# Optimization experiments

Measured on AMD Instinct MI355X. Metric: run time of the kernel, lower is better.

## Reference

```python
import jax, jax.numpy as jnp
import numpy as np


def _mlp2(x, w1, b1, w2, b2):
    # two-linear MLP with tanh after each layer (Sequential(MLP, activation))
    h = jnp.tanh(x @ w1.T + b1)
    return jnp.tanh(h @ w2.T + b2)


def setup_inputs() -> dict:
    key = jax.random.key(0)
    ks = jax.random.split(key, 12)
    N, K, D, H, C = 20000, 32, 128, 128, 64
    s = 0.1
    return {
        "z": jax.random.normal(ks[0], (N, D), jnp.float32),
        "z_": jax.random.normal(ks[1], (N, K, D), jnp.float32),
        "cur_w1": s * jax.random.normal(ks[2], (H, D), jnp.float32),
        "cur_b1": jax.random.uniform(ks[3], (H,), jnp.float32, -0.1, 0.1),
        "cur_w2": s * jax.random.normal(ks[4], (H, H), jnp.float32),
        "cur_b2": jax.random.uniform(ks[5], (H,), jnp.float32, -0.1, 0.1),
        "nbr_w1": s * jax.random.normal(ks[6], (H, 2 * D), jnp.float32),
        "nbr_b1": jax.random.uniform(ks[7], (H,), jnp.float32, -0.1, 0.1),
        "nbr_w2": s * jax.random.normal(ks[8], (H, H), jnp.float32),
        "nbr_b2": jax.random.uniform(ks[9], (H,), jnp.float32, -0.1, 0.1),
        "out_w": s * jax.random.normal(ks[10], (C, 2 * H), jnp.float32),
        "out_b": jax.random.uniform(ks[11], (C,), jnp.float32, -0.1, 0.1),
    }


def reference(z, z_, cur_w1, cur_b1, cur_w2, cur_b2,
              nbr_w1, nbr_b1, nbr_w2, nbr_b2, out_w, out_b):
    N, K, D = z_.shape
    # current-node branch: [N, H]
    v = _mlp2(z, cur_w1, cur_b1, cur_w2, cur_b2)
    # neighbor branch: repeat z over K, concat with z_ -> [N, K, 2D]
    zc = jnp.concatenate([jnp.broadcast_to(z[:, None, :], (N, K, D)), z_], axis=2)
    vn = _mlp2(zc, nbr_w1, nbr_b1, nbr_w2, nbr_b2)  # [N, K, H]
    v_ = vn.sum(axis=1)  # sum-aggregate over neighbors -> [N, H]
    # output linear on concatenated features -> [N, dim_c]
    dc = jnp.concatenate([v, v_], axis=1) @ out_w.T + out_b
    return dc
```

## Files before the change

### kernel.cpp

```cpp
#include <hip/hip_runtime.h>


typedef __bf16 bf16;
typedef __bf16 bf16x2 __attribute__((ext_vector_type(2)));
typedef __bf16 bf16x4 __attribute__((ext_vector_type(4)));
typedef __bf16 bf16x8 __attribute__((ext_vector_type(8)));
typedef float  f32x4  __attribute__((ext_vector_type(4)));

#define MFMA(a, b, c) __builtin_amdgcn_mfma_f32_16x16x32_bf16((a), (b), (c), 0, 0, 0)

#define C2LOG2E 2.885390081777927f

__device__ __forceinline__ void block_sync_lds() {
    asm volatile("s_waitcnt lgkmcnt(0)\n\ts_barrier" ::: "memory");
}

__device__ __forceinline__ float fast_tanh(float x) {
    float t = __builtin_amdgcn_exp2f(x * C2LOG2E);
    return 1.0f - 2.0f * __builtin_amdgcn_rcpf(t + 1.0f);
}
__device__ __forceinline__ float fast_tanh_fb(float acc, float uc) {
    float t = __builtin_amdgcn_exp2f(__builtin_fmaf(acc, C2LOG2E, uc));
    return 1.0f - 2.0f * __builtin_amdgcn_rcpf(t + 1.0f);
}
__device__ __forceinline__ float tanh_rpart(float acc, float uc) {
    float t = __builtin_amdgcn_exp2f(__builtin_fmaf(acc, C2LOG2E, uc));
    return __builtin_amdgcn_rcpf(t + 1.0f);
}

__device__ __forceinline__ bf16x8 cvt8(f32x4 a, f32x4 b) {
    bf16x8 r;
    r[0] = (bf16)a[0]; r[1] = (bf16)a[1]; r[2] = (bf16)a[2]; r[3] = (bf16)a[3];
    r[4] = (bf16)b[0]; r[5] = (bf16)b[1]; r[6] = (bf16)b[2]; r[7] = (bf16)b[3];
    return r;
}

__device__ __forceinline__ int swz128(int row, int col) {
    int c = (col >> 3) ^ (row & 15);
    return row * 256 + c * 16 + (col & 7) * 2;
}
__device__ __forceinline__ int swz256(int row, int col) {
    int c = (col >> 3) ^ (row & 15);
    return row * 512 + c * 16 + (col & 7) * 2;
}

__device__ __forceinline__ void st_pair(char* base, int off, float a, float b) {
    bf16x2 p = {(bf16)a, (bf16)b};
    *(bf16x2*)(base + off) = p;
}

__global__ __launch_bounds__(256, 2) void nbr_kernel(
    const float* __restrict__ zn, const float* __restrict__ u1,
    const float* __restrict__ w1, const float* __restrict__ w2,
    const float* __restrict__ b2,
    bf16* __restrict__ feat, int NP)
{
    __shared__ char zc_lds[2][32 * 256];
    __shared__ char h1_lds[2][32 * 256];

    const int t = threadIdx.x;
    const int wv = t >> 6, lane = t & 63, g = lane >> 4, li = lane & 15;
    const int hbase = wv * 32;

    bf16x8 w1f[2][4];
#pragma unroll
    for (int ht = 0; ht < 2; ++ht)
#pragma unroll
        for (int kb = 0; kb < 4; ++kb) {
            const float* p = w1 + (size_t)(hbase + 16*ht + li) * 256 + 128 + kb*32 + 8*g;
            w1f[ht][kb] = cvt8(*(const f32x4*)p, *(const f32x4*)(p + 4));
        }
    bf16x8 w2f[2][4];
#pragma unroll
    for (int nt = 0; nt < 2; ++nt)
#pragma unroll
        for (int kb = 0; kb < 4; ++kb) {
            const float* p = w2 + (size_t)(hbase + 16*nt + li) * 128 + kb*32 + 8*g;
            w2f[nt][kb] = cvt8(*(const f32x4*)p, *(const f32x4*)(p + 4));
        }
    float bc2v[2];
#pragma unroll
    for (int nt = 0; nt < 2; ++nt) bc2v[nt] = b2[hbase + 16*nt + li] * C2LOG2E;

    const int sm  = t >> 3;
    const int scf = (t & 7) * 16;
    const int str = gridDim.x;

    f32x4 rA[2][4], rB[2][4];
    f32x4 uu[2][2];

    auto load_zn = [&](f32x4 (&R)[2][4], int pp) {
#pragma unroll
        for (int j = 0; j < 2; ++j) {
            const float* src = zn + ((size_t)(2*pp + j) * 32 + sm) * 128 + scf;
#pragma unroll
            for (int q = 0; q < 4; ++q) R[j][q] = *(const f32x4*)(src + 4*q);
        }
    };
    auto load_u = [&](int pp) {
#pragma unroll
        for (int j = 0; j < 2; ++j)
#pragma unroll
            for (int ht = 0; ht < 2; ++ht)
                uu[j][ht] = *(const f32x4*)(u1 + (size_t)(2*pp + j) * 128 + hbase + 16*ht + 4*g);
    };

    const int p0 = blockIdx.x;
    load_zn(rA, p0);
    if (p0 + str < NP) load_zn(rB, p0 + str);
    load_u(p0);

    const f32x4 vzero = {0.f, 0.f, 0.f, 0.f};

    auto iter_body = [&](f32x4 (&R)[2][4], int p) {
#pragma unroll
        for (int j = 0; j < 2; ++j) {
            *(bf16x8*)(zc_lds[j] + swz128(sm, scf))     = cvt8(R[j][0], R[j][1]);
            *(bf16x8*)(zc_lds[j] + swz128(sm, scf + 8)) = cvt8(R[j][2], R[j][3]);
        }
        block_sync_lds();

        const int pz = p + 2*str;
        if (pz < NP) load_zn(R, pz);

        f32x4 acc1[2][2][2];
#pragma unroll
        for (int j = 0; j < 2; ++j)
#pragma unroll
            for (int a = 0; a < 2; ++a)
#pragma unroll
                for (int b = 0; b < 2; ++b) acc1[j][a][b] = vzero;

        __builtin_amdgcn_s_setprio(1);
#pragma unroll
        for (int kb = 0; kb < 4; ++kb) {
            bf16x8 bz[2][2];
#pragma unroll
            for (int j = 0; j < 2; ++j)
#pragma unroll
                for (int mt = 0; mt < 2; ++mt)
                    bz[j][mt] = *(const bf16x8*)(zc_lds[j] + swz128(16*mt + li, kb*32 + 8*g));
#pragma unroll
            for (int j = 0; j < 2; ++j)
#pragma unroll
                for (int ht = 0; ht < 2; ++ht)
#pragma unroll
                    for (int mt = 0; mt < 2; ++mt)
                        acc1[j][ht][mt] = MFMA(w1f[ht][kb], bz[j][mt], acc1[j][ht][mt]);
        }
        __builtin_amdgcn_s_setprio(0);

#pragma unroll
        for (int j = 0; j < 2; ++j)
#pragma unroll
            for (int ht = 0; ht < 2; ++ht) {
                f32x4 uc = uu[j][ht] * C2LOG2E;
#pragma unroll
                for (int mt = 0; mt < 2; ++mt) {
                    float v0 = fast_tanh_fb(acc1[j][ht][mt][0], uc[0]);
                    float v1 = fast_tanh_fb(acc1[j][ht][mt][1], uc[1]);
                    float v2 = fast_tanh_fb(acc1[j][ht][mt][2], uc[2]);
                    float v3 = fast_tanh_fb(acc1[j][ht][mt][3], uc[3]);
                    int m = 16*mt + li;
                    int h = hbase + 16*ht + 4*g;
                    bf16x4 q = {(bf16)v0, (bf16)v1, (bf16)v2, (bf16)v3};
                    *(bf16x4*)(h1_lds[j] + swz128(m, h)) = q;
                }
            }

        const int pu = p + str;
        if (pu < NP) load_u(pu);
        block_sync_lds();

        f32x4 acc2[2][2][2];
#pragma unroll
        for (int j = 0; j < 2; ++j)
#pragma unroll
            for (int a = 0; a < 2; ++a)
#pragma unroll
                for (int b = 0; b < 2; ++b) acc2[j][a][b] = vzero;

        __builtin_amdgcn_s_setprio(1);
#pragma unroll
        for (int kb = 0; kb < 4; ++kb) {
            bf16x8 ah[2][2];
#pragma unroll
            for (int j = 0; j < 2; ++j)
#pragma unroll
                for (int mt = 0; mt < 2; ++mt)
                    ah[j][mt] = *(const bf16x8*)(h1_lds[j] + swz128(16*mt + li, kb*32 + 8*g));
#pragma unroll
            for (int j = 0; j < 2; ++j)
#pragma unroll
                for (int mt = 0; mt < 2; ++mt)
#pragma unroll
                    for (int nt = 0; nt < 2; ++nt)
                        acc2[j][mt][nt] = MFMA(ah[j][mt], w2f[nt][kb], acc2[j][mt][nt]);
        }
        __builtin_amdgcn_s_setprio(0);

#pragma unroll
        for (int j = 0; j < 2; ++j) {
            float sr0 = 0.f, sr1 = 0.f;
#pragma unroll
            for (int mt = 0; mt < 2; ++mt)
#pragma unroll
                for (int rr = 0; rr < 4; ++rr) {
                    sr0 += tanh_rpart(acc2[j][mt][0][rr], bc2v[0]);
                    sr1 += tanh_rpart(acc2[j][mt][1][rr], bc2v[1]);
                }
            sr0 += __shfl_xor(sr0, 16); sr0 += __shfl_xor(sr0, 32);
            sr1 += __shfl_xor(sr1, 16); sr1 += __shfl_xor(sr1, 32);
            if (lane < 16) {
                float s0 = __builtin_fmaf(-2.f, sr0, 32.f);
                float s1 = __builtin_fmaf(-2.f, sr1, 32.f);
                bf16* dst = feat + (size_t)(2*p + j) * 256 + 128 + hbase + lane;
                dst[0]  = (bf16)s0;
                dst[16] = (bf16)s1;
            }
        }
    };

    for (int p = p0; p < NP; ) {
        iter_body(rA, p);
        p += str;
        if (p >= NP) break;
        iter_body(rB, p);
        p += str;
    }
}

__global__ __launch_bounds__(256, 2) void cur_kernel(
    const float* __restrict__ z,
    const float* __restrict__ w1, const float* __restrict__ b1,
    const float* __restrict__ w2, const float* __restrict__ b2,
    const float* __restrict__ nw1, const float* __restrict__ nb1,
    bf16* __restrict__ feat, float* __restrict__ u1, int N)
{
    __shared__ char z_lds[64 * 256];
    __shared__ char h1_lds[64 * 256];

    const int t = threadIdx.x;
    const int wv = t >> 6, lane = t & 63, g = lane >> 4, li = lane & 15;
    const int hbase = wv * 32;
    const int n0 = blockIdx.x * 64;

    bf16x8 w1f[2][4], w2f[2][4], wzf[2][4];
#pragma unroll
    for (int ht = 0; ht < 2; ++ht)
#pragma unroll
        for (int kb = 0; kb < 4; ++kb) {
            const float* p1 = w1 + (size_t)(hbase + 16*ht + li) * 128 + kb*32 + 8*g;
            w1f[ht][kb] = cvt8(*(const f32x4*)p1, *(const f32x4*)(p1 + 4));
            const float* p2 = w2 + (size_t)(hbase + 16*ht + li) * 128 + kb*32 + 8*g;
            w2f[ht][kb] = cvt8(*(const f32x4*)p2, *(const f32x4*)(p2 + 4));
            const float* p3 = nw1 + (size_t)(hbase + 16*ht + li) * 256 + kb*32 + 8*g;
            wzf[ht][kb] = cvt8(*(const f32x4*)p3, *(const f32x4*)(p3 + 4));
        }
    float b1v[2][4], b2v[2][4], bnv[2][4];
#pragma unroll
    for (int ht = 0; ht < 2; ++ht)
#pragma unroll
        for (int rr = 0; rr < 4; ++rr) {
            b1v[ht][rr] = b1[hbase + 16*ht + 4*g + rr];
            b2v[ht][rr] = b2[hbase + 16*ht + 4*g + rr];
            bnv[ht][rr] = nb1[hbase + 16*ht + 4*g + rr];
        }

    {
        int m = t >> 2;
        int c0 = (t & 3) * 32;
        int row = n0 + m; if (row > N - 1) row = N - 1;
        const float* src = z + (size_t)row * 128 + c0;
#pragma unroll
        for (int q = 0; q < 4; ++q) {
            f32x4 a = *(const f32x4*)(src + 8*q);
            f32x4 b = *(const f32x4*)(src + 8*q + 4);
            *(bf16x8*)(z_lds + swz128(m, c0 + 8*q)) = cvt8(a, b);
        }
    }
    __syncthreads();

    const f32x4 vzero = {0.f, 0.f, 0.f, 0.f};
    f32x4 acc1[2][4], accz[2][4];
#pragma unroll
    for (int a = 0; a < 2; ++a)
#pragma unroll
        for (int b = 0; b < 4; ++b) { acc1[a][b] = vzero; accz[a][b] = vzero; }

#pragma unroll
    for (int kb = 0; kb < 4; ++kb) {
        bf16x8 bz[4];
#pragma unroll
        for (int mt = 0; mt < 4; ++mt)
            bz[mt] = *(const bf16x8*)(z_lds + swz128(16*mt + li, kb*32 + 8*g));
#pragma unroll
        for (int ht = 0; ht < 2; ++ht)
#pragma unroll
            for (int mt = 0; mt < 4; ++mt) {
                acc1[ht][mt] = MFMA(w1f[ht][kb], bz[mt], acc1[ht][mt]);
                accz[ht][mt] = MFMA(wzf[ht][kb], bz[mt], accz[ht][mt]);
            }
    }

#pragma unroll
    for (int ht = 0; ht < 2; ++ht)
#pragma unroll
        for (int mt = 0; mt < 4; ++mt) {
            int row = n0 + 16*mt + li;
            if (row < N) {
                f32x4 v;
#pragma unroll
                for (int rr = 0; rr < 4; ++rr) v[rr] = accz[ht][mt][rr] + bnv[ht][rr];
                *(f32x4*)(u1 + (size_t)row * 128 + hbase + 16*ht + 4*g) = v;
            }
        }

#pragma unroll
    for (int ht = 0; ht < 2; ++ht)
#pragma unroll
        for (int mt = 0; mt < 4; ++mt) {
            float v0 = fast_tanh(acc1[ht][mt][0] + b1v[ht][0]);
            float v1 = fast_tanh(acc1[ht][mt][1] + b1v[ht][1]);
            float v2 = fast_tanh(acc1[ht][mt][2] + b1v[ht][2]);
            float v3 = fast_tanh(acc1[ht][mt][3] + b1v[ht][3]);
            int m = 16*mt + li;
            int h = hbase + 16*ht + 4*g;
            st_pair(h1_lds, swz128(m, h),     v0, v1);
            st_pair(h1_lds, swz128(m, h + 2), v2, v3);
        }
    __syncthreads();

    f32x4 acc2[2][4];
#pragma unroll
    for (int a = 0; a < 2; ++a)
#pragma unroll
        for (int b = 0; b < 4; ++b) acc2[a][b] = vzero;

#pragma unroll
    for (int kb = 0; kb < 4; ++kb) {
        bf16x8 bh[4];
#pragma unroll
        for (int mt = 0; mt < 4; ++mt)
            bh[mt] = *(const bf16x8*)(h1_lds + swz128(16*mt + li, kb*32 + 8*g));
#pragma unroll
        for (int ht = 0; ht < 2; ++ht)
#pragma unroll
            for (int mt = 0; mt < 4; ++mt)
                acc2[ht][mt] = MFMA(w2f[ht][kb], bh[mt], acc2[ht][mt]);
    }
#pragma unroll
    for (int ht = 0; ht < 2; ++ht)
#pragma unroll
        for (int mt = 0; mt < 4; ++mt) {
            float v0 = fast_tanh(acc2[ht][mt][0] + b2v[ht][0]);
            float v1 = fast_tanh(acc2[ht][mt][1] + b2v[ht][1]);
            float v2 = fast_tanh(acc2[ht][mt][2] + b2v[ht][2]);
            float v3 = fast_tanh(acc2[ht][mt][3] + b2v[ht][3]);
            int row = n0 + 16*mt + li;
            if (row < N) {
                int h = hbase + 16*ht + 4*g;
                bf16* dst = feat + (size_t)row * 256 + h;
                bf16x2 p01 = {(bf16)v0, (bf16)v1};
                bf16x2 p23 = {(bf16)v2, (bf16)v3};
                *(bf16x2*)(dst)     = p01;
                *(bf16x2*)(dst + 2) = p23;
            }
        }
}

__global__ __launch_bounds__(256, 2) void out_kernel(
    const bf16* __restrict__ feat,
    const float* __restrict__ ow, const float* __restrict__ ob,
    float* __restrict__ out, int N)
{
    __shared__ char f_lds[64 * 512];

    const int t = threadIdx.x, wv = t >> 6, lane = t & 63, g = lane >> 4, li = lane & 15;
    const int cbase = wv * 16;
    const int n0 = blockIdx.x * 64;

    bf16x8 owf[8];
#pragma unroll
    for (int kb = 0; kb < 8; ++kb) {
        const float* p = ow + (size_t)(cbase + li) * 256 + kb*32 + 8*g;
        owf[kb] = cvt8(*(const f32x4*)p, *(const f32x4*)(p + 4));
    }
    float obv = ob[cbase + li];

    {
        int m = t >> 2;
        int c0 = (t & 3) * 64;
        int row = n0 + m; if (row > N - 1) row = N - 1;
        const bf16* src = feat + (size_t)row * 256 + c0;
#pragma unroll
        for (int q = 0; q < 8; ++q)
            *(bf16x8*)(f_lds + swz256(m, c0 + 8*q)) = *(const bf16x8*)(src + 8*q);
    }
    __syncthreads();

    const f32x4 vzero = {0.f, 0.f, 0.f, 0.f};
    f32x4 acc[4];
#pragma unroll
    for (int a = 0; a < 4; ++a) acc[a] = vzero;

#pragma unroll
    for (int kb = 0; kb < 8; ++kb) {
        bf16x8 af[4];
#pragma unroll
        for (int mt = 0; mt < 4; ++mt)
            af[mt] = *(const bf16x8*)(f_lds + swz256(16*mt + li, kb*32 + 8*g));
#pragma unroll
        for (int mt = 0; mt < 4; ++mt)
            acc[mt] = MFMA(af[mt], owf[kb], acc[mt]);
    }
#pragma unroll
    for (int mt = 0; mt < 4; ++mt)
#pragma unroll
        for (int rr = 0; rr < 4; ++rr) {
            int row = n0 + 16*mt + 4*g + rr;
            if (row < N) out[(size_t)row * 64 + cbase + li] = acc[mt][rr] + obv;
        }
}

extern "C" void kernel_launch(void* const* d_in, const int* in_sizes, int n_in,
                              void* d_out, int out_size, void* d_ws, size_t ws_size,
                              hipStream_t stream) {
    const float* z   = (const float*)d_in[0];
    const float* zn  = (const float*)d_in[1];
    const float* cw1 = (const float*)d_in[2];
    const float* cb1 = (const float*)d_in[3];
    const float* cw2 = (const float*)d_in[4];
    const float* cb2 = (const float*)d_in[5];
    const float* nw1 = (const float*)d_in[6];
    const float* nb1 = (const float*)d_in[7];
    const float* nw2 = (const float*)d_in[8];
    const float* nb2 = (const float*)d_in[9];
    const float* ow  = (const float*)d_in[10];
    const float* ob  = (const float*)d_in[11];
    float* out = (float*)d_out;

    const int N  = in_sizes[0] / 128;
    const int NP = N / 2;
    const int nblk = (N + 63) / 64;

    bf16*  feat = (bf16*)d_ws;
    float* u1   = (float*)((char*)d_ws + (size_t)N * 256 * sizeof(bf16));

    (void)n_in; (void)out_size; (void)ws_size;

    cur_kernel<<<nblk, 256, 0, stream>>>(z, cw1, cb1, cw2, cb2, nw1, nb1, feat, u1, N);
    nbr_kernel<<<512, 256, 0, stream>>>(zn, u1, nw1, nw2, nb2, feat, NP);
    out_kernel<<<nblk, 256, 0, stream>>>(feat, ow, ob, out, N);
}
```

Baseline: 129.2 us.

## Shrink neighbor prefetch depth to raise occupancy to three blocks per CU

The neighbor kernel now prefetches only one node-pair ahead, split into two chunks issued at different points in the iteration, instead of double-buffering two full pairs in registers. This roughly halves the prefetch register footprint. In exchange, launch bounds rise to 3 blocks per CU and the grid grows from 512 to 768 blocks. The trade is less per-wave latency hiding from prefetch in return for more resident waves hiding latency.

```diff
diff --git a/kernel.cpp b/kernel.cpp
--- a/kernel.cpp
+++ b/kernel.cpp
@@ -49,7 +49,7 @@
     *(bf16x2*)(base + off) = p;
 }
 
-__global__ __launch_bounds__(256, 2) void nbr_kernel(
+__global__ __launch_bounds__(256, 3) void nbr_kernel(
     const float* __restrict__ zn, const float* __restrict__ u1,
     const float* __restrict__ w1, const float* __restrict__ w2,
     const float* __restrict__ b2,
@@ -78,24 +78,21 @@
             const float* p = w2 + (size_t)(hbase + 16*nt + li) * 128 + kb*32 + 8*g;
             w2f[nt][kb] = cvt8(*(const f32x4*)p, *(const f32x4*)(p + 4));
         }
-    float bc2v[2];
-#pragma unroll
-    for (int nt = 0; nt < 2; ++nt) bc2v[nt] = b2[hbase + 16*nt + li] * C2LOG2E;
+    float bc2[2];
+#pragma unroll
+    for (int nt = 0; nt < 2; ++nt) bc2[nt] = b2[hbase + 16*nt + li] * C2LOG2E;
 
     const int sm  = t >> 3;
     const int scf = (t & 7) * 16;
     const int str = gridDim.x;
 
-    f32x4 rA[2][4], rB[2][4];
+    f32x4 rA[4], rB[4];
     f32x4 uu[2][2];
 
-    auto load_zn = [&](f32x4 (&R)[2][4], int pp) {
-#pragma unroll
-        for (int j = 0; j < 2; ++j) {
-            const float* src = zn + ((size_t)(2*pp + j) * 32 + sm) * 128 + scf;
-#pragma unroll
-            for (int q = 0; q < 4; ++q) R[j][q] = *(const f32x4*)(src + 4*q);
-        }
+    auto load_chunk = [&](f32x4 (&R)[4], int nidx) {
+        const float* src = zn + ((size_t)nidx * 32 + sm) * 128 + scf;
+#pragma unroll
+        for (int q = 0; q < 4; ++q) R[q] = *(const f32x4*)(src + 4*q);
     };
     auto load_u = [&](int pp) {
 #pragma unroll
@@ -105,23 +102,24 @@
                 uu[j][ht] = *(const f32x4*)(u1 + (size_t)(2*pp + j) * 128 + hbase + 16*ht + 4*g);
     };
 
-    const int p0 = blockIdx.x;
-    load_zn(rA, p0);
-    if (p0 + str < NP) load_zn(rB, p0 + str);
-    load_u(p0);
+    {
+        const int p0 = blockIdx.x;
+        load_chunk(rA, 2*p0);
+        load_chunk(rB, 2*p0 + 1);
+        load_u(p0);
+    }
 
     const f32x4 vzero = {0.f, 0.f, 0.f, 0.f};
 
-    auto iter_body = [&](f32x4 (&R)[2][4], int p) {
-#pragma unroll
-        for (int j = 0; j < 2; ++j) {
-            *(bf16x8*)(zc_lds[j] + swz128(sm, scf))     = cvt8(R[j][0], R[j][1]);
-            *(bf16x8*)(zc_lds[j] + swz128(sm, scf + 8)) = cvt8(R[j][2], R[j][3]);
-        }
+    for (int p = blockIdx.x; p < NP; p += str) {
+        *(bf16x8*)(zc_lds[0] + swz128(sm, scf))     = cvt8(rA[0], rA[1]);
+        *(bf16x8*)(zc_lds[0] + swz128(sm, scf + 8)) = cvt8(rA[2], rA[3]);
+        *(bf16x8*)(zc_lds[1] + swz128(sm, scf))     = cvt8(rB[0], rB[1]);
+        *(bf16x8*)(zc_lds[1] + swz128(sm, scf + 8)) = cvt8(rB[2], rB[3]);
         block_sync_lds();
 
-        const int pz = p + 2*str;
-        if (pz < NP) load_zn(R, pz);
+        const int pp = p + str;
+        if (pp < NP) load_chunk(rA, 2*pp);
 
         f32x4 acc1[2][2][2];
 #pragma unroll
@@ -157,19 +155,18 @@
                 f32x4 uc = uu[j][ht] * C2LOG2E;
 #pragma unroll
                 for (int mt = 0; mt < 2; ++mt) {
-                    float v0 = fast_tanh_fb(acc1[j][ht][mt][0], uc[0]);
-                    float v1 = fast_tanh_fb(acc1[j][ht][mt][1], uc[1]);
-                    float v2 = fast_tanh_fb(acc1[j][ht][mt][2], uc[2]);
-                    float v3 = fast_tanh_fb(acc1[j][ht][mt][3], uc[3]);
-                    int m = 16*mt + li;
-                    int h = hbase + 16*ht + 4*g;
-                    bf16x4 q = {(bf16)v0, (bf16)v1, (bf16)v2, (bf16)v3};
-                    *(bf16x4*)(h1_lds[j] + swz128(m, h)) = q;
+                    bf16x4 q;
+#pragma unroll
+                    for (int r = 0; r < 4; ++r)
+                        q[r] = (bf16)fast_tanh_fb(acc1[j][ht][mt][r], uc[r]);
+                    *(bf16x4*)(h1_lds[j] + swz128(16*mt + li, hbase + 16*ht + 4*g)) = q;
                 }
             }
 
-        const int pu = p + str;
-        if (pu < NP) load_u(pu);
+        if (pp < NP) {
+            load_chunk(rB, 2*pp + 1);
+            load_u(pp);
+        }
         block_sync_lds();
 
         f32x4 acc2[2][2][2];
@@ -206,8 +203,8 @@
             for (int mt = 0; mt < 2; ++mt)
 #pragma unroll
                 for (int rr = 0; rr < 4; ++rr) {
-                    sr0 += tanh_rpart(acc2[j][mt][0][rr], bc2v[0]);
-                    sr1 += tanh_rpart(acc2[j][mt][1][rr], bc2v[1]);
+                    sr0 += tanh_rpart(acc2[j][mt][0][rr], bc2[0]);
+                    sr1 += tanh_rpart(acc2[j][mt][1][rr], bc2[1]);
                 }
             sr0 += __shfl_xor(sr0, 16); sr0 += __shfl_xor(sr0, 32);
             sr1 += __shfl_xor(sr1, 16); sr1 += __shfl_xor(sr1, 32);
@@ -219,14 +216,6 @@
                 dst[16] = (bf16)s1;
             }
         }
-    };
-
-    for (int p = p0; p < NP; ) {
-        iter_body(rA, p);
-        p += str;
-        if (p >= NP) break;
-        iter_body(rB, p);
-        p += str;
     }
 }
 
@@ -444,12 +433,13 @@
     const int NP = N / 2;
     const int nblk = (N + 63) / 64;
 
-    bf16*  feat = (bf16*)d_ws;
-    float* u1   = (float*)((char*)d_ws + (size_t)N * 256 * sizeof(bf16));
+    char* ws = (char*)d_ws;
+    bf16*  feat = (bf16*)ws;
+    float* u1   = (float*)(ws + (size_t)N * 256 * sizeof(bf16));
 
     (void)n_in; (void)out_size; (void)ws_size;
 
     cur_kernel<<<nblk, 256, 0, stream>>>(z, cw1, cb1, cw2, cb2, nw1, nb1, feat, u1, N);
-    nbr_kernel<<<512, 256, 0, stream>>>(zn, u1, nw1, nw2, nb2, feat, NP);
+    nbr_kernel<<<768, 256, 0, stream>>>(zn, u1, nw1, nw2, nb2, feat, NP);
     out_kernel<<<nblk, 256, 0, stream>>>(feat, ow, ob, out, N);
 }
```

Result: slower. 150.4 us (+16.4%).
